# Optimization experiments

Hardware: AMD Instinct MI355X
Metric: run time of the kernel (lower is better)

The kernel has to match this reference:

```python
import jax, jax.numpy as jnp
import numpy as np

NUM_CLASSES = 50000
NUM_SAMPLED = 1000
D_MODEL = 1024
BATCH, SEQ = 32, 512


def _log_expected_count(ids, num_sampled, num_classes):
    # TF log-uniform candidate sampler (unique=True):
    # P(c) = log((c+2)/(c+1)) / log(num_classes+1)
    # E[count] = -expm1(num_sampled * log1p(-P))
    ids_f = ids.astype(jnp.float32)
    p = (jnp.log(ids_f + 2.0) - jnp.log(ids_f + 1.0)) / np.float32(np.log(num_classes + 1.0))
    return jnp.log(-jnp.expm1(num_sampled * jnp.log1p(-p)))


def setup_inputs() -> dict:
    key = jax.random.key(0)
    k1, k2, k3, k4 = jax.random.split(key, 4)
    lstm_outputs = jax.random.normal(k1, (BATCH, SEQ, D_MODEL), dtype=jnp.float32)
    next_token_ids = jax.random.randint(k2, (BATCH, SEQ), 0, NUM_CLASSES)
    sampled_ids = jax.random.randint(k3, (BATCH, NUM_SAMPLED), 0, NUM_CLASSES)
    W = jax.random.normal(k4, (NUM_CLASSES, D_MODEL), dtype=jnp.float32) * (1.0 / np.sqrt(D_MODEL))
    b = jnp.zeros((NUM_CLASSES,), dtype=jnp.float32)
    return {"lstm_outputs": lstm_outputs, "next_token_ids": next_token_ids,
            "sampled_ids": sampled_ids, "W": W, "b": b}


def reference(lstm_outputs, next_token_ids, sampled_ids, W, b):
    # Vectorized sampled-softmax loss (tf.nn.sampled_softmax_loss with
    # log-uniform sampler, partition_strategy irrelevant, accidental-hit removal),
    # mapped over the batch dim as the original tf.map_fn does.
    log_q_true = _log_expected_count(next_token_ids, NUM_SAMPLED, NUM_CLASSES)   # [B,T]
    log_q_samp = _log_expected_count(sampled_ids, NUM_SAMPLED, NUM_CLASSES)      # [B,S]

    w_true = W[next_token_ids]                                                   # [B,T,D]
    true_logit = (jnp.einsum('btd,btd->bt', lstm_outputs, w_true)
                  + b[next_token_ids] - log_q_true)                              # [B,T]

    w_samp = W[sampled_ids]                                                      # [B,S,D]
    samp_logits = (jnp.einsum('btd,bsd->bts', lstm_outputs, w_samp)
                   + b[sampled_ids][:, None, :] - log_q_samp[:, None, :])        # [B,T,S]

    # remove accidental hits (sampled id == true label)
    hit = sampled_ids[:, None, :] == next_token_ids[:, :, None]                  # [B,T,S]
    samp_logits = jnp.where(hit, jnp.float32(-1e9), samp_logits)

    all_logits = jnp.concatenate([true_logit[..., None], samp_logits], axis=-1)  # [B,T,1+S]
    # softmax CE with true class at index 0
    losses = jax.nn.logsumexp(all_logits, axis=-1) - true_logit                  # [B,T]
    return 0.5 * jnp.mean(losses)
```

## Files before the change

### kernel.cpp

```cpp
#include <hip/hip_runtime.h>
#include <cmath>

#define BATCH 32
#define SEQLEN 512
#define NSAMP 1000
#define DMODEL 1024
#define NCHUNK 4

typedef __bf16 bf16x8_t __attribute__((ext_vector_type(8)));
typedef float f32x4_t __attribute__((ext_vector_type(4)));

__device__ __forceinline__ unsigned pack_bf2(float lo, float hi) {
    unsigned ulo = __float_as_uint(lo);
    unsigned uhi = __float_as_uint(hi);
    ulo = (ulo + 0x7fffu + ((ulo >> 16) & 1u)) >> 16;
    uhi = (uhi + 0x7fffu + ((uhi >> 16) & 1u)) & 0xffff0000u;
    return (ulo & 0xffffu) | uhi;
}

__device__ __forceinline__ float log_expected_count(int id) {
    float idf = (float)id;
    float p = log1pf(1.0f / (idf + 1.0f)) * 0.09242316f;
    return logf(-expm1f(1000.0f * log1pf(-p)));
}

__device__ __forceinline__ void gl16(const void* g, void* l) {
    __builtin_amdgcn_global_load_lds(
        (const __attribute__((address_space(1))) unsigned int*)g,
        (__attribute__((address_space(3))) unsigned int*)l,
        16, 0, 0);
}

__global__ __launch_bounds__(256) void prep_kernel(
    const float* __restrict__ h, const int* __restrict__ labels,
    const int* __restrict__ sids, const float* __restrict__ W,
    const float* __restrict__ bias, unsigned short* __restrict__ Wb,
    unsigned short* __restrict__ hb,
    float* __restrict__ adjw, float* __restrict__ tlw)
{
    const int w = threadIdx.x >> 6, lane = threadIdx.x & 63;
    if (blockIdx.x < 8000) {
        const int row = blockIdx.x * 4 + w;
        const int sv = sids[row];
        const float4* src = (const float4*)(W + (size_t)sv * DMODEL);
        unsigned short* dst = Wb + (size_t)row * DMODEL;
#pragma unroll
        for (int j = 0; j < 4; ++j) {
            float4 v = src[lane + j * 64];
            uint2 u;
            u.x = pack_bf2(v.x, v.y);
            u.y = pack_bf2(v.z, v.w);
            *(uint2*)(dst + (lane + j * 64) * 4) = u;
        }
        if (lane == 0) adjw[row] = bias[sv] - log_expected_count(sv);
    } else {
        const int r = (blockIdx.x - 8000) * 4 + w;
        const int lab = labels[r];
        const float4* hp = (const float4*)(h + (size_t)r * DMODEL);
        const float4* wp = (const float4*)(W + (size_t)lab * DMODEL);
        unsigned short* hdst = hb + (size_t)r * DMODEL;
        float s = 0.0f;
#pragma unroll
        for (int j = 0; j < 4; ++j) {
            float4 a = hp[lane + j * 64];
            float4 c = wp[lane + j * 64];
            s += a.x * c.x + a.y * c.y + a.z * c.z + a.w * c.w;
            uint2 u;
            u.x = pack_bf2(a.x, a.y);
            u.y = pack_bf2(a.z, a.w);
            *(uint2*)(hdst + (lane + j * 64) * 4) = u;
        }
#pragma unroll
        for (int off = 32; off > 0; off >>= 1) s += __shfl_xor(s, off, 64);
        if (lane == 0) tlw[r] = s + bias[lab] - log_expected_count(lab);
    }
}

__global__ __launch_bounds__(256, 2) void sampled_softmax_main(
    const int* __restrict__ labels, const int* __restrict__ sids,
    const unsigned short* __restrict__ hb, const unsigned short* __restrict__ Wb,
    const float* __restrict__ adjw,
    float* __restrict__ pm, float* __restrict__ pl)
{
    __shared__ __align__(16) unsigned short Ab[3][64 * 32];
    __shared__ __align__(16) unsigned short Bb[3][256 * 32];
    __shared__ int   sid_lds[256];
    __shared__ float adj_lds[256];
    __shared__ int   lab_lds[64];
    __shared__ float mpart[4][64];
    __shared__ float lpart[4][64];

    const int bb     = blockIdx.x;
    const int chunk  = blockIdx.y;
    const int tile_t = blockIdx.z;
    const int t0  = tile_t * 64;
    const int tid = threadIdx.x;
    const int w   = tid >> 6, l = tid & 63;
    const int lm  = l & 15,   q = l >> 4;
    const int rl4 = l >> 2,  cp = l & 3;

    {
        const int s = chunk * 256 + tid;
        const bool v = s < NSAMP;
        sid_lds[tid] = v ? sids[bb * NSAMP + s] : -1;
        adj_lds[tid] = v ? adjw[bb * NSAMP + s] : 0.0f;
        if (tid < 64) lab_lds[tid] = labels[bb * SEQLEN + t0 + tid];
    }

    const int swzs = (rl4 & 3) ^ ((rl4 >> 2) & 3);
    const int cs = (cp ^ swzs) * 8;
    const unsigned short* aS = hb + (size_t)(bb * SEQLEN + t0 + 16 * w + rl4) * DMODEL + cs;
    const unsigned short* bS[4];
#pragma unroll
    for (int j = 0; j < 4; ++j) {
        int rb = chunk * 256 + 64 * w + 16 * j + rl4;
        if (rb > NSAMP - 1) rb = NSAMP - 1;
        bS[j] = Wb + (size_t)(bb * NSAMP + rb) * DMODEL + cs;
    }

#define STAGE_TILE(KT, BUF)                                                   \
    do {                                                                      \
        const int _adv = (KT) * 32;                                           \
        gl16(aS + _adv, &Ab[BUF][(16 * w) * 32]);                             \
        gl16(bS[0] + _adv, &Bb[BUF][(64 * w) * 32]);                          \
        gl16(bS[1] + _adv, &Bb[BUF][(64 * w + 16) * 32]);                     \
        gl16(bS[2] + _adv, &Bb[BUF][(64 * w + 32) * 32]);                     \
        gl16(bS[3] + _adv, &Bb[BUF][(64 * w + 48) * 32]);                     \
    } while (0)

    const int fswz = (lm & 3) ^ ((lm >> 2) & 3);
    const int fp = (q ^ fswz) * 8;
    int aoff[4], boff[4];
#pragma unroll
    for (int t = 0; t < 4; ++t) aoff[t] = (16 * t + lm) * 32 + fp;
#pragma unroll
    for (int c = 0; c < 4; ++c) boff[c] = (64 * w + 16 * c + lm) * 32 + fp;

    f32x4_t acc[4][4];
#pragma unroll
    for (int t = 0; t < 4; ++t)
#pragma unroll
        for (int c = 0; c < 4; ++c) acc[t][c] = (f32x4_t){0.f, 0.f, 0.f, 0.f};

    STAGE_TILE(0, 0);
    STAGE_TILE(1, 1);
    asm volatile("s_waitcnt lgkmcnt(0)" ::: "memory");
    __builtin_amdgcn_s_barrier();

#pragma unroll
    for (int kt = 0; kt < 32; ++kt) {
        if (kt < 31) { asm volatile("s_waitcnt vmcnt(5)" ::: "memory"); }
        else         { asm volatile("s_waitcnt vmcnt(0)" ::: "memory"); }
        __builtin_amdgcn_s_barrier();
        if (kt + 2 < 32) STAGE_TILE(kt + 2, (kt + 2) % 3);

        const unsigned short* Ac = Ab[kt % 3];
        const unsigned short* Bc = Bb[kt % 3];
        bf16x8_t fa[4];
#pragma unroll
        for (int t = 0; t < 4; ++t) fa[t] = *(const bf16x8_t*)(Ac + aoff[t]);
        bf16x8_t fb[4];
#pragma unroll
        for (int c = 0; c < 4; ++c) fb[c] = *(const bf16x8_t*)(Bc + boff[c]);
        __builtin_amdgcn_s_setprio(1);
#pragma unroll
        for (int c = 0; c < 4; ++c)
#pragma unroll
            for (int t = 0; t < 4; ++t)
                acc[t][c] = __builtin_amdgcn_mfma_f32_16x16x32_bf16(fa[t], fb[c], acc[t][c], 0, 0, 0);
        __builtin_amdgcn_s_setprio(0);
    }
#undef STAGE_TILE

    float adjv[4]; int sidv[4]; bool cval[4];
#pragma unroll
    for (int c = 0; c < 4; ++c) {
        const int col = 64 * w + 16 * c + lm;
        adjv[c] = adj_lds[col];
        sidv[c] = sid_lds[col];
        cval[c] = (chunk * 256 + col) < NSAMP;
    }
#pragma unroll
    for (int t = 0; t < 4; ++t) {
#pragma unroll
        for (int i = 0; i < 4; ++i) {
            const int r = 16 * t + 4 * q + i;
            const int lab = lab_lds[r];
            float x[4]; bool ok[4];
            float m = -INFINITY;
#pragma unroll
            for (int c = 0; c < 4; ++c) {
                x[c] = acc[t][c][i] + adjv[c];
                ok[c] = cval[c] && (sidv[c] != lab);
                if (ok[c]) m = fmaxf(m, x[c]);
            }
            float ls = 0.0f;
#pragma unroll
            for (int c = 0; c < 4; ++c) ls += ok[c] ? __expf(x[c] - m) : 0.0f;
#pragma unroll
            for (int off = 1; off < 16; off <<= 1) {
                const float mo = __shfl_xor(m, off, 64);
                const float lo = __shfl_xor(ls, off, 64);
                const float M  = fmaxf(m, mo);
                const float e1 = (ls > 0.0f) ? ls * __expf(m - M) : 0.0f;
                const float e2 = (lo > 0.0f) ? lo * __expf(mo - M) : 0.0f;
                m = M; ls = e1 + e2;
            }
            if (lm == 0) { mpart[w][r] = m; lpart[w][r] = ls; }
        }
    }
    __syncthreads();
    if (tid < 64) {
        float m = -INFINITY, lsum = 0.0f;
#pragma unroll
        for (int p = 0; p < 4; ++p) {
            const float mp = mpart[p][tid];
            const float lp = lpart[p][tid];
            if (lp > 0.0f) {
                if (mp > m) { lsum = lsum * __expf(m - mp) + lp; m = mp; }
                else        { lsum += lp * __expf(mp - m); }
            }
        }
        const int idx = (bb * SEQLEN + t0 + tid) * NCHUNK + chunk;
        pm[idx] = m;
        pl[idx] = lsum;
    }
}

__global__ __launch_bounds__(256) void combine_kernel(
    const float* __restrict__ pm, const float* __restrict__ pl,
    const float* __restrict__ tlw, float* __restrict__ bsum)
{
    __shared__ float wsum[4];
    const int tid = threadIdx.x;
    const int w = tid >> 6, lane = tid & 63;
    const int idx = blockIdx.x * 256 + tid;
    float m = -INFINITY, l = 0.0f;
#pragma unroll
    for (int c = 0; c < NCHUNK; ++c) {
        const float mp = pm[idx * NCHUNK + c];
        const float lp = pl[idx * NCHUNK + c];
        if (lp > 0.0f) {
            if (mp > m) { l = l * __expf(m - mp) + lp; m = mp; }
            else        { l += lp * __expf(mp - m); }
        }
    }
    const float t = tlw[idx];
    const float M = fmaxf(m, t);
    float loss = __logf(l * __expf(m - M) + __expf(t - M)) + M - t;
#pragma unroll
    for (int off = 32; off > 0; off >>= 1) loss += __shfl_xor(loss, off, 64);
    if (lane == 0) wsum[w] = loss;
    __syncthreads();
    if (tid == 0) bsum[blockIdx.x] = wsum[0] + wsum[1] + wsum[2] + wsum[3];
}

__global__ void finalize_kernel(const float* __restrict__ bsum, float* __restrict__ out) {
    float v = bsum[threadIdx.x];
#pragma unroll
    for (int off = 32; off > 0; off >>= 1) v += __shfl_xor(v, off, 64);
    if (threadIdx.x == 0) out[0] = v * (0.5f / (float)(BATCH * SEQLEN));
}

extern "C" void kernel_launch(void* const* d_in, const int* in_sizes, int n_in,
                              void* d_out, int out_size, void* d_ws, size_t ws_size,
                              hipStream_t stream) {
    const float* h      = (const float*)d_in[0];
    const int*   labels = (const int*)d_in[1];
    const int*   sids   = (const int*)d_in[2];
    const float* W      = (const float*)d_in[3];
    const float* bias   = (const float*)d_in[4];

    char* base = (char*)d_ws;
    unsigned short* Wb = (unsigned short*)base;
    unsigned short* hb = (unsigned short*)(base + 65536000);
    float* adjw = (float*)(base + 99090432);
    float* tlw  = (float*)(base + 99218432);
    float* pmw  = (float*)(base + 99283968);
    float* plw  = (float*)(base + 99546112);
    float* bsum = (float*)(base + 99808256);

    prep_kernel<<<dim3(12096), dim3(256), 0, stream>>>(h, labels, sids, W, bias, Wb, hb, adjw, tlw);
    sampled_softmax_main<<<dim3(32, NCHUNK, 8), dim3(256), 0, stream>>>(
        labels, sids, hb, Wb, adjw, pmw, plw);
    combine_kernel<<<dim3(64), dim3(256), 0, stream>>>(pmw, plw, tlw, bsum);
    finalize_kernel<<<dim3(1), dim3(64), 0, stream>>>(bsum, (float*)d_out);
}
```

Baseline: 407.7 us.

## Enlarge GEMM tile to 256x256 with 8 waves per workgroup

```diff
diff --git a/kernel.cpp b/kernel.cpp
--- a/kernel.cpp
+++ b/kernel.cpp
@@ -76,69 +76,71 @@
     }
 }
 
-__global__ __launch_bounds__(256, 2) void sampled_softmax_main(
+__global__ __launch_bounds__(512, 2) void sampled_softmax_main(
     const int* __restrict__ labels, const int* __restrict__ sids,
     const unsigned short* __restrict__ hb, const unsigned short* __restrict__ Wb,
     const float* __restrict__ adjw,
     float* __restrict__ pm, float* __restrict__ pl)
 {
-    __shared__ __align__(16) unsigned short Ab[3][64 * 32];
+    __shared__ __align__(16) unsigned short Ab[3][256 * 32];
     __shared__ __align__(16) unsigned short Bb[3][256 * 32];
     __shared__ int   sid_lds[256];
     __shared__ float adj_lds[256];
-    __shared__ int   lab_lds[64];
-    __shared__ float mpart[4][64];
-    __shared__ float lpart[4][64];
-
-    const int bb     = blockIdx.x;
-    const int chunk  = blockIdx.y;
-    const int tile_t = blockIdx.z;
-    const int t0  = tile_t * 64;
+    __shared__ int   lab_lds[256];
+    __shared__ float mpart[4][256];
+    __shared__ float lpart[4][256];
+
+    const int wg     = blockIdx.x;
+    const int bb     = wg & 31;
+    const int rest   = wg >> 5;
+    const int tile_t = rest & 1;
+    const int chunk  = rest >> 1;
+    const int t0  = tile_t * 256;
     const int tid = threadIdx.x;
-    const int w   = tid >> 6, l = tid & 63;
-    const int lm  = l & 15,   q = l >> 4;
+    const int wv  = tid >> 6, l = tid & 63;
+    const int wr  = wv >> 2, wc = wv & 3;
+    const int lm  = l & 15,  q = l >> 4;
     const int rl4 = l >> 2,  cp = l & 3;
 
-    {
+    if (tid < 256) {
         const int s = chunk * 256 + tid;
         const bool v = s < NSAMP;
         sid_lds[tid] = v ? sids[bb * NSAMP + s] : -1;
         adj_lds[tid] = v ? adjw[bb * NSAMP + s] : 0.0f;
-        if (tid < 64) lab_lds[tid] = labels[bb * SEQLEN + t0 + tid];
+        lab_lds[tid] = labels[bb * SEQLEN + t0 + tid];
     }
 
     const int swzs = (rl4 & 3) ^ ((rl4 >> 2) & 3);
     const int cs = (cp ^ swzs) * 8;
-    const unsigned short* aS = hb + (size_t)(bb * SEQLEN + t0 + 16 * w + rl4) * DMODEL + cs;
-    const unsigned short* bS[4];
-#pragma unroll
-    for (int j = 0; j < 4; ++j) {
-        int rb = chunk * 256 + 64 * w + 16 * j + rl4;
-        if (rb > NSAMP - 1) rb = NSAMP - 1;
-        bS[j] = Wb + (size_t)(bb * NSAMP + rb) * DMODEL + cs;
-    }
+    const unsigned short* aS0 = hb + (size_t)(bb * SEQLEN + t0 + 32 * wv + rl4) * DMODEL + cs;
+    const unsigned short* aS1 = aS0 + (size_t)16 * DMODEL;
+    int rb0 = chunk * 256 + 32 * wv + rl4;
+    int rb1 = rb0 + 16;
+    if (rb0 > NSAMP - 1) rb0 = NSAMP - 1;
+    if (rb1 > NSAMP - 1) rb1 = NSAMP - 1;
+    const unsigned short* bS0 = Wb + (size_t)(bb * NSAMP + rb0) * DMODEL + cs;
+    const unsigned short* bS1 = Wb + (size_t)(bb * NSAMP + rb1) * DMODEL + cs;
 
 #define STAGE_TILE(KT, BUF)                                                   \
     do {                                                                      \
         const int _adv = (KT) * 32;                                           \
-        gl16(aS + _adv, &Ab[BUF][(16 * w) * 32]);                             \
-        gl16(bS[0] + _adv, &Bb[BUF][(64 * w) * 32]);                          \
-        gl16(bS[1] + _adv, &Bb[BUF][(64 * w + 16) * 32]);                     \
-        gl16(bS[2] + _adv, &Bb[BUF][(64 * w + 32) * 32]);                     \
-        gl16(bS[3] + _adv, &Bb[BUF][(64 * w + 48) * 32]);                     \
+        gl16(aS0 + _adv, &Ab[BUF][(32 * wv) * 32]);                           \
+        gl16(aS1 + _adv, &Ab[BUF][(32 * wv + 16) * 32]);                      \
+        gl16(bS0 + _adv, &Bb[BUF][(32 * wv) * 32]);                           \
+        gl16(bS1 + _adv, &Bb[BUF][(32 * wv + 16) * 32]);                      \
     } while (0)
 
     const int fswz = (lm & 3) ^ ((lm >> 2) & 3);
     const int fp = (q ^ fswz) * 8;
-    int aoff[4], boff[4];
-#pragma unroll
-    for (int t = 0; t < 4; ++t) aoff[t] = (16 * t + lm) * 32 + fp;
-#pragma unroll
-    for (int c = 0; c < 4; ++c) boff[c] = (64 * w + 16 * c + lm) * 32 + fp;
-
-    f32x4_t acc[4][4];
-#pragma unroll
-    for (int t = 0; t < 4; ++t)
+    int aoff[8], boff[4];
+#pragma unroll
+    for (int t = 0; t < 8; ++t) aoff[t] = (128 * wr + 16 * t + lm) * 32 + fp;
+#pragma unroll
+    for (int c = 0; c < 4; ++c) boff[c] = (64 * wc + 16 * c + lm) * 32 + fp;
+
+    f32x4_t acc[8][4];
+#pragma unroll
+    for (int t = 0; t < 8; ++t)
 #pragma unroll
         for (int c = 0; c < 4; ++c) acc[t][c] = (f32x4_t){0.f, 0.f, 0.f, 0.f};
 
@@ -149,25 +151,24 @@
 
 #pragma unroll
     for (int kt = 0; kt < 32; ++kt) {
-        if (kt < 31) { asm volatile("s_waitcnt vmcnt(5)" ::: "memory"); }
+        if (kt < 31) { asm volatile("s_waitcnt vmcnt(4)" ::: "memory"); }
         else         { asm volatile("s_waitcnt vmcnt(0)" ::: "memory"); }
         __builtin_amdgcn_s_barrier();
         if (kt + 2 < 32) STAGE_TILE(kt + 2, (kt + 2) % 3);
 
         const unsigned short* Ac = Ab[kt % 3];
         const unsigned short* Bc = Bb[kt % 3];
-        bf16x8_t fa[4];
-#pragma unroll
-        for (int t = 0; t < 4; ++t) fa[t] = *(const bf16x8_t*)(Ac + aoff[t]);
-        bf16x8_t fb[4];
-#pragma unroll
-        for (int c = 0; c < 4; ++c) fb[c] = *(const bf16x8_t*)(Bc + boff[c]);
+        bf16x8_t fa[8];
+#pragma unroll
+        for (int t = 0; t < 8; ++t) fa[t] = *(const bf16x8_t*)(Ac + aoff[t]);
         __builtin_amdgcn_s_setprio(1);
 #pragma unroll
-        for (int c = 0; c < 4; ++c)
-#pragma unroll
-            for (int t = 0; t < 4; ++t)
-                acc[t][c] = __builtin_amdgcn_mfma_f32_16x16x32_bf16(fa[t], fb[c], acc[t][c], 0, 0, 0);
+        for (int c = 0; c < 4; ++c) {
+            bf16x8_t fb = *(const bf16x8_t*)(Bc + boff[c]);
+#pragma unroll
+            for (int t = 0; t < 8; ++t)
+                acc[t][c] = __builtin_amdgcn_mfma_f32_16x16x32_bf16(fa[t], fb, acc[t][c], 0, 0, 0);
+        }
         __builtin_amdgcn_s_setprio(0);
     }
 #undef STAGE_TILE
@@ -175,16 +176,16 @@
     float adjv[4]; int sidv[4]; bool cval[4];
 #pragma unroll
     for (int c = 0; c < 4; ++c) {
-        const int col = 64 * w + 16 * c + lm;
+        const int col = 64 * wc + 16 * c + lm;
         adjv[c] = adj_lds[col];
         sidv[c] = sid_lds[col];
         cval[c] = (chunk * 256 + col) < NSAMP;
     }
 #pragma unroll
-    for (int t = 0; t < 4; ++t) {
+    for (int t = 0; t < 8; ++t) {
 #pragma unroll
         for (int i = 0; i < 4; ++i) {
-            const int r = 16 * t + 4 * q + i;
+            const int r = 128 * wr + 16 * t + 4 * q + i;
             const int lab = lab_lds[r];
             float x[4]; bool ok[4];
             float m = -INFINITY;
@@ -206,11 +207,11 @@
                 const float e2 = (lo > 0.0f) ? lo * __expf(mo - M) : 0.0f;
                 m = M; ls = e1 + e2;
             }
-            if (lm == 0) { mpart[w][r] = m; lpart[w][r] = ls; }
+            if (lm == 0) { mpart[wc][r] = m; lpart[wc][r] = ls; }
         }
     }
     __syncthreads();
-    if (tid < 64) {
+    if (tid < 256) {
         float m = -INFINITY, lsum = 0.0f;
 #pragma unroll
         for (int p = 0; p < 4; ++p) {
@@ -281,7 +282,7 @@
     float* bsum = (float*)(base + 99808256);
 
     prep_kernel<<<dim3(12096), dim3(256), 0, stream>>>(h, labels, sids, W, bias, Wb, hb, adjw, tlw);
-    sampled_softmax_main<<<dim3(32, NCHUNK, 8), dim3(256), 0, stream>>>(
+    sampled_softmax_main<<<dim3(256), dim3(512), 0, stream>>>(
         labels, sids, hb, Wb, adjw, pmw, plw);
     combine_kernel<<<dim3(64), dim3(256), 0, stream>>>(pmw, plw, tlw, bsum);
     finalize_kernel<<<dim3(1), dim3(64), 0, stream>>>(bsum, (float*)d_out);
```

New measurement: 394.8 us. 3.2% less time.
